# Optimization experiments

Hardware: AMD Instinct MI355X
Metric: run time of the kernel (lower is better)

## Reference

```python
import jax, jax.numpy as jnp
import numpy as np

# ---- sign binarization with straight-through estimator (standard BNN) ----
@jax.custom_vjp
def binarize(x):
    return jnp.where(x >= 0, 1.0, -1.0).astype(x.dtype)

def _bin_fwd(x):
    return binarize(x), x

def _bin_bwd(x, g):
    return (g * (jnp.abs(x) <= 1.0).astype(g.dtype),)

binarize.defvjp(_bin_fwd, _bin_bwd)

def conv2d(x, w):
    # x: [N,C,H,W], w: [O,I,kh,kw], stride 1, VALID padding (padding=0)
    return jax.lax.conv_general_dilated(
        x, w, window_strides=(1, 1), padding='VALID',
        dimension_numbers=('NCHW', 'OIHW', 'NCHW'))

def maxpool2(x):
    return jax.lax.reduce_window(x, -jnp.inf, jax.lax.max,
                                 (1, 1, 2, 2), (1, 1, 2, 2), 'VALID')

def hardtanh(x):
    return jnp.clip(x, -1.0, 1.0)

def setup_inputs() -> dict:
    key = jax.random.key(0)
    ks = jax.random.split(key, 11)
    B = 8192
    s = 0.1
    return {
        'x':   jax.random.normal(ks[0], (B, 3, 32, 32), jnp.float32),
        'w1':  jax.random.normal(ks[1], (6, 3, 5, 5), jnp.float32) * s,
        'b1':  jax.random.normal(ks[2], (6,), jnp.float32) * s,
        'w2':  jax.random.normal(ks[3], (16, 6, 5, 5), jnp.float32) * s,
        'b2':  jax.random.normal(ks[4], (16,), jnp.float32) * s,
        'wf1': jax.random.normal(ks[5], (120, 400), jnp.float32) * s,
        'bf1': jax.random.normal(ks[6], (120,), jnp.float32) * s,
        'wf2': jax.random.normal(ks[7], (84, 120), jnp.float32) * s,
        'bf2': jax.random.normal(ks[8], (84,), jnp.float32) * s,
        'wf3': jax.random.normal(ks[9], (10, 84), jnp.float32) * s,
        'bf3': jax.random.normal(ks[10], (10,), jnp.float32) * s,
    }

def reference(x, w1, b1, w2, b2, wf1, bf1, wf2, bf2, wf3, bf3):
    # conv1: first layer -> real-valued input, binarized weights
    out = conv2d(x, binarize(w1)) + b1[None, :, None, None]   # [B,6,28,28]
    out = maxpool2(hardtanh(out))                              # [B,6,14,14]
    # conv2: binarized input and weights
    out = conv2d(binarize(out), binarize(w2)) + b2[None, :, None, None]  # [B,16,10,10]
    out = maxpool2(hardtanh(out))                              # [B,16,5,5]
    out = out.reshape(out.shape[0], -1)                        # [B,400]
    out = hardtanh(binarize(out) @ binarize(wf1).T + bf1)      # [B,120]
    out = hardtanh(binarize(out) @ binarize(wf2).T + bf2)      # [B,84]
    out = binarize(out) @ binarize(wf3).T + bf3                # [B,10]
    return out
```

## Files before the change

kernel.cpp:

```cpp
#include <hip/hip_runtime.h>
#include <stdint.h>

#define TPB 256
#define RCAP 128
#define BAND 0.05f

#define WS_BFR   0
#define WS_W1B   1280
#define WS_W2PK  1298
#define WS_WF1P  1378
#define WS_WF2PK 4378
#define WS_WF3PK 4714

typedef _Float16 half8 __attribute__((ext_vector_type(8)));
typedef float f32x4 __attribute__((ext_vector_type(4)));
typedef unsigned int u32x4 __attribute__((ext_vector_type(4)));

__device__ __forceinline__ uint32_t pkf16(float a, float b) {
  uint32_t lo = (uint32_t)__builtin_bit_cast(uint16_t, (_Float16)a);
  uint32_t hi = (uint32_t)__builtin_bit_cast(uint16_t, (_Float16)b);
  return lo | (hi << 16);
}

__device__ __forceinline__ double win_sum(const float* __restrict__ xb,
                                          uint32_t b0, uint32_t b1, uint32_t b2) {
  double s = 0.0;
#pragma unroll
  for (int ic = 0; ic < 3; ++ic)
#pragma unroll
    for (int rr = 0; rr < 5; ++rr) {
      const float* rp = xb + ic * 1024 + rr * 32;
#pragma unroll
      for (int kc = 0; kc < 5; ++kc) {
        const int idx = ic * 25 + rr * 5 + kc;
        const uint32_t bw = (idx < 32) ? b0 : ((idx < 64) ? b1 : b2);
        double xv = (double)rp[kc];
        s += ((bw >> (idx & 31)) & 1u) ? xv : -xv;
      }
    }
  return s;
}

__global__ __launch_bounds__(TPB) void prep_kernel(
    const float* __restrict__ w1, const float* __restrict__ w2,
    const float* __restrict__ wf1, const float* __restrict__ wf2,
    const float* __restrict__ wf3, uint32_t* __restrict__ wsu)
{
  int id = blockIdx.x * TPB + threadIdx.x;
  if (id < 1280) {
    int s = id >> 8, r = id & 255, ln = r >> 2, dw = r & 3;
    int g4 = ln >> 4, n = ln & 15;
    int o = 4 * s + g4, r6 = o / 3, cp = o % 3;
    int c = n >> 1, dy = n & 1;
    uint32_t w = 0;
    for (int h = 0; h < 2; ++h) {
      int j2 = dw * 2 + h;
      int ic = j2 & 3, pix = j2 >> 2, kc = cp * 2 + pix, kr = r6 - dy;
      uint32_t f = 0;
      if (n < 12 && o < 18 && ic < 3 && kc < 5 && kr >= 0 && kr <= 4)
        f = (w1[(c * 3 + ic) * 25 + kr * 5 + kc] >= 0.f) ? 0x3C00u : 0xBC00u;
      w |= f << (16 * h);
    }
    wsu[WS_BFR + id] = w;
  } else if (id < 1298) {
    int i = id - 1280, c = i / 3, q = i % 3;
    uint32_t w = 0;
    for (int b = 0; b < 32; ++b) {
      int k = q * 32 + b;
      if (k < 75) w |= (uint32_t)(w1[c*75 + k] >= 0.f) << b;
    }
    wsu[WS_W1B + i] = w;
  } else if (id < 1378) {
    int r = id - 1298, oc = r / 5, kr = r % 5;
    uint32_t w = 0;
    for (int c = 0; c < 6; ++c)
      for (int k = 0; k < 5; ++k)
        w |= (uint32_t)(w2[((oc*6 + c)*5 + kr)*5 + k] >= 0.f) << (5*c + k);
    wsu[WS_W2PK + r] = w;
  } else if (id < 4378) {
    int r = id - 1378, o = r / 25, p = r % 25;
    uint32_t w = 0;
    for (int oc = 0; oc < 16; ++oc)
      w |= (uint32_t)(wf1[o*400 + oc*25 + p] >= 0.f) << oc;
    wsu[WS_WF1P + r] = w;
  } else if (id < 4714) {
    int r = id - 4378, o = r / 4, q = r % 4;
    uint32_t w = 0;
    for (int b = 0; b < 32; ++b) {
      int n = q*32 + b;
      if (n < 120) w |= (uint32_t)(wf2[o*120 + n] >= 0.f) << b;
    }
    wsu[WS_WF2PK + r] = w;
  } else if (id < 4744) {
    int r = id - 4714, o = r / 3, q = r % 3;
    uint32_t w = 0;
    for (int b = 0; b < 32; ++b) {
      int n = q*32 + b;
      if (n < 84) w |= (uint32_t)(wf3[o*84 + n] >= 0.f) << b;
    }
    wsu[WS_WF3PK + r] = w;
  }
}

__global__ void __launch_bounds__(TPB, 4) lenet_kernel(
    const float* __restrict__ x,
    const float* __restrict__ b1, const float* __restrict__ b2,
    const float* __restrict__ bf1, const float* __restrict__ bf2,
    const float* __restrict__ bf3,
    const uint32_t* __restrict__ wsu,
    float* __restrict__ out, int imgs_total)
{
  __shared__ __align__(16) union Ovl {
    uint32_t imgh[8448];
    uint32_t ppatch[4][10][10][5];
  } ovl;
  __shared__ uint32_t w1bs[18];
  __shared__ float sb1[6];
  __shared__ float sb2[16];
  __shared__ uint32_t bits1[4][6][14];
  __shared__ uint32_t border_[4][6][14];
  __shared__ uint32_t w2pks[16][5];
  __shared__ uint32_t bits2[4][25];
  __shared__ uint32_t wf2pks[84][4];
  __shared__ uint32_t wf3pks[10][3];
  __shared__ uint32_t bitsf1[4][4];
  __shared__ uint32_t bitsf2[4][3];
  __shared__ uint32_t rlist[RCAP];
  __shared__ int rcnt;

  const int t = threadIdx.x;
  const int lane = t & 63;
  const int wv = t >> 6;
  const int m16 = lane & 15;
  const int g4 = lane >> 4;
  const long long img0 = (long long)blockIdx.x * 4;
  const int nimg = (img0 + 4 <= imgs_total) ? 4 : (int)(imgs_total - img0);

  {
    const int im = t >> 6, y = (t >> 1) & 31, xh = t & 1;
    if (im < nimg) {
      const float* rp = x + (img0 + im) * 3072 + y * 32 + xh * 16;
      const int pixbase = (im * 32 + y) * 33 + xh * 16;
#pragma unroll
      for (int q = 0; q < 4; ++q) {
        float4 f0 = *(const float4*)(rp +    0 + 4 * q);
        float4 f1 = *(const float4*)(rp + 1024 + 4 * q);
        float4 f2 = *(const float4*)(rp + 2048 + 4 * q);
        uint32_t* d = &ovl.imgh[2 * (pixbase + 4 * q)];
        *(uint2*)(d + 0) = make_uint2(pkf16(f0.x, f1.x), pkf16(f2.x, 0.f));
        *(uint2*)(d + 2) = make_uint2(pkf16(f0.y, f1.y), pkf16(f2.y, 0.f));
        *(uint2*)(d + 4) = make_uint2(pkf16(f0.z, f1.z), pkf16(f2.z, 0.f));
        *(uint2*)(d + 6) = make_uint2(pkf16(f0.w, f1.w), pkf16(f2.w, 0.f));
      }
    }
    for (int id = t; id < 128; id += TPB) {
      int i2 = id >> 5, yy = id & 31;
      *(uint2*)&ovl.imgh[2 * ((i2 * 32 + yy) * 33 + 32)] = make_uint2(0u, 0u);
    }
    if (t < 18) w1bs[t] = wsu[WS_W1B + t];
    if (t < 6)  sb1[t] = b1[t];
    if (t >= 8 && t < 24) sb2[t - 8] = b2[t - 8];
    if (t < 80) w2pks[t / 5][t % 5] = wsu[WS_W2PK + t];
    if (t < 168) {
      ((uint32_t*)wf2pks)[t]       = wsu[WS_WF2PK + t];
      ((uint32_t*)wf2pks)[t + 168] = wsu[WS_WF2PK + t + 168];
    }
    if (t < 30) ((uint32_t*)wf3pks)[t] = wsu[WS_WF3PK + t];
    for (int id = t; id < 336; id += TPB) {
      ((uint32_t*)bits1)[id] = 0; ((uint32_t*)border_)[id] = 0;
    }
    if (t < 100) ((uint32_t*)bits2)[t] = 0;
    if (t < 16) ((uint32_t*)bitsf1)[t] = 0;
    if (t < 12) ((uint32_t*)bitsf2)[t] = 0;
    if (t == 0) rcnt = 0;
  }
  __syncthreads();

  if (wv < nimg) {
    u32x4 bf[5];
#pragma unroll
    for (int s = 0; s < 5; ++s)
      bf[s] = *(const u32x4*)&wsu[WS_BFR + (s << 8) + (lane << 2)];
    int koffs[5];
#pragma unroll
    for (int s = 0; s < 5; ++s) {
      const int o = 4 * s + g4;
      koffs[s] = (o < 18) ? (o / 3) * 33 + (o % 3) * 2 : 0;
    }
    const int n = m16;
    const int c = n >> 1;
    const float bcr = sb1[(n < 12) ? c : 0];
    for (int pyi = 0; pyi < 14; ++pyi) {
      const int rowpix = (wv * 32 + 2 * pyi) * 33 + m16;
      f32x4 aX = {0.f, 0.f, 0.f, 0.f}, aY = {0.f, 0.f, 0.f, 0.f};
#pragma unroll
      for (int s = 0; s < 5; ++s) {
        const uint2* pX = (const uint2*)&ovl.imgh[2 * (rowpix + koffs[s])];
        const uint2* pY = (const uint2*)&ovl.imgh[2 * (rowpix + 12 + koffs[s])];
        uint2 x0 = pX[0], x1 = pX[1];
        uint2 y0 = pY[0], y1 = pY[1];
        u32x4 wa = {x0.x, x0.y, x1.x, x1.y};
        u32x4 wb = {y0.x, y0.y, y1.x, y1.y};
        aX = __builtin_amdgcn_mfma_f32_16x16x32_f16(
               __builtin_bit_cast(half8, wa), __builtin_bit_cast(half8, bf[s]), aX, 0, 0, 0);
        aY = __builtin_amdgcn_mfma_f32_16x16x32_f16(
               __builtin_bit_cast(half8, wb), __builtin_bit_cast(half8, bf[s]), aY, 0, 0, 0);
      }
      float pX0 = fmaxf(aX[0], aX[1]), pX1 = fmaxf(aX[2], aX[3]);
      float pY0 = fmaxf(aY[0], aY[1]), pY1 = fmaxf(aY[2], aY[3]);
      float qX0 = fmaxf(pX0, __shfl_xor(pX0, 1));
      float qX1 = fmaxf(pX1, __shfl_xor(pX1, 1));
      float qY0 = fmaxf(pY0, __shfl_xor(pY0, 1));
      float qY1 = fmaxf(pY1, __shfl_xor(pY1, 1));
      uint32_t comb = 0;
      {
        float v0 = qX0 + bcr, v1 = qX1 + bcr, v2 = qY0 + bcr, v3 = qY1 + bcr;
        const int p0 = g4 * 2, p1 = g4 * 2 + 1, p2 = 6 + g4 * 2, p3 = 7 + g4 * 2;
        if (fabsf(v0) < BAND) comb |= 1u << (16 + p0); else if (v0 >= 0.f) comb |= 1u << p0;
        if (fabsf(v1) < BAND) comb |= 1u << (16 + p1); else if (v1 >= 0.f) comb |= 1u << p1;
        if (fabsf(v2) < BAND) comb |= 1u << (16 + p2); else if (v2 >= 0.f) comb |= 1u << p2;
        if (fabsf(v3) < BAND) comb |= 1u << (16 + p3); else if (v3 >= 0.f) comb |= 1u << p3;
      }
      comb |= __shfl_xor(comb, 16);
      comb |= __shfl_xor(comb, 32);
      if (g4 == 0 && n < 12 && (n & 1) == 0) {
        bits1[wv][c][pyi]   = comb & 0x3FFFu;
        border_[wv][c][pyi] = comb >> 16;
      }
    }
  }
  __syncthreads();

  for (int id = t; id < 336; id += TPB) {
    uint32_t bw = ((uint32_t*)border_)[id];
    while (bw) {
      int pj = __ffs(bw) - 1;
      bw &= bw - 1;
      int slot = atomicAdd(&rcnt, 1);
      if (slot < RCAP) rlist[slot] = (uint32_t)(id * 16 + pj);
    }
  }
  __syncthreads();

  {
    const int cnt = min(rcnt, RCAP);
    for (int k = t; k < cnt * 4; k += TPB) {
      const int e = k >> 2, win = k & 3;
      const uint32_t ent = rlist[e];
      const int pj = ent & 15, w = ent >> 4;
      const int pi = w % 14, c = (w / 14) % 6, im = w / 84;
      const int dr = win >> 1, dc = win & 1;
      const float* xb = x + (img0 + im) * 3072 + (2*pi + dr) * 32 + (2*pj + dc);
      double s = win_sum(xb, w1bs[c*3], w1bs[c*3+1], w1bs[c*3+2]);
      double s1 = fmax(s, __shfl_xor(s, 1));
      double sm = fmax(s1, __shfl_xor(s1, 2));
      if (win == 0) {
        if (sm + (double)sb1[c] >= 0.0)
          atomicOr(&((uint32_t*)bits1)[w], 1u << pj);
      }
    }
    if (rcnt > RCAP) {
      for (int id = t; id < 4704; id += TPB) {
        const int w = id / 14, pj = id % 14;
        if ((((uint32_t*)border_)[w] >> pj) & 1u) {
          const int pi = w % 14, c = (w / 14) % 6, im = w / 84;
          double best = -1e300;
          for (int dr = 0; dr < 2; ++dr)
            for (int dc = 0; dc < 2; ++dc) {
              const float* xb = x + (img0 + im) * 3072 + (2*pi + dr) * 32 + (2*pj + dc);
              double s = win_sum(xb, w1bs[c*3], w1bs[c*3+1], w1bs[c*3+2]);
              best = best > s ? best : s;
            }
          if (best + (double)sb1[c] >= 0.0)
            atomicOr(&((uint32_t*)bits1)[w], 1u << pj);
        }
      }
    }
  }
  __syncthreads();

  for (int id = t; id < 2000; id += TPB) {
    const int im  = id / 500;
    const int rem = id % 500;
    const int kr = rem % 5;
    const int ij = rem / 5;
    const int i = ij / 10, j = ij % 10;
    uint32_t w = 0;
#pragma unroll
    for (int c = 0; c < 6; ++c)
      w |= ((bits1[im][c][i + kr] >> j) & 31u) << (5*c);
    ovl.ppatch[im][i][j][kr] = w;
  }
  __syncthreads();

  for (int id = t; id < 1600; id += TPB) {
    const int im  = id / 400;
    const int rem = id % 400;
    const int oc  = rem / 25;
    const int pos = rem % 25;
    const int pi = pos / 5, pj = pos % 5;
    int dmin = 1000;
#pragma unroll
    for (int dy = 0; dy < 2; ++dy)
#pragma unroll
      for (int dx = 0; dx < 2; ++dx) {
        const uint32_t* pp = ovl.ppatch[im][2*pi + dy][2*pj + dx];
        int d = 0;
#pragma unroll
        for (int kr = 0; kr < 5; ++kr) d += __popc(pp[kr] ^ w2pks[oc][kr]);
        dmin = min(dmin, d);
      }
    float v = (float)(150 - 2*dmin) + sb2[oc];
    if (v >= 0.f) atomicOr(&bits2[im][pos], 1u << oc);
  }
  __syncthreads();

  for (int id = t; id < 480; id += TPB) {
    const int im = id / 120;
    const int o = id % 120;
    const uint32_t* wrow = wsu + WS_WF1P + o*25;
    int d = 0;
#pragma unroll
    for (int p = 0; p < 25; ++p) d += __popc(bits2[im][p] ^ wrow[p]);
    float v = (float)(400 - 2*d) + bf1[o];
    if (v >= 0.f) atomicOr(&bitsf1[im][o >> 5], 1u << (o & 31));
  }
  __syncthreads();

  for (int id = t; id < 336; id += TPB) {
    const int im = id / 84;
    const int o = id % 84;
    int d = 0;
#pragma unroll
    for (int q = 0; q < 4; ++q) d += __popc(bitsf1[im][q] ^ wf2pks[o][q]);
    float v = (float)(120 - 2*d) + bf2[o];
    if (v >= 0.f) atomicOr(&bitsf2[im][o >> 5], 1u << (o & 31));
  }
  __syncthreads();

  for (int id = t; id < 40; id += TPB) {
    const int im = id / 10;
    const int o = id % 10;
    if (im < nimg) {
      int d = 0;
#pragma unroll
      for (int q = 0; q < 3; ++q) d += __popc(bitsf2[im][q] ^ wf3pks[o][q]);
      out[(img0 + im)*10 + o] = (float)(84 - 2*d) + bf3[o];
    }
  }
}

extern "C" void kernel_launch(void* const* d_in, const int* in_sizes, int n_in,
                              void* d_out, int out_size, void* d_ws, size_t ws_size,
                              hipStream_t stream)
{
  const float* x   = (const float*)d_in[0];
  const float* w1  = (const float*)d_in[1];
  const float* b1  = (const float*)d_in[2];
  const float* w2  = (const float*)d_in[3];
  const float* b2  = (const float*)d_in[4];
  const float* wf1 = (const float*)d_in[5];
  const float* bf1 = (const float*)d_in[6];
  const float* wf2 = (const float*)d_in[7];
  const float* bf2 = (const float*)d_in[8];
  const float* wf3 = (const float*)d_in[9];
  const float* bf3 = (const float*)d_in[10];
  uint32_t* wsu = (uint32_t*)d_ws;

  const int imgs = in_sizes[0] / 3072;
  hipLaunchKernelGGL(prep_kernel, dim3(19), dim3(TPB), 0, stream,
                     w1, w2, wf1, wf2, wf3, wsu);
  const int nblk = (imgs + 3) / 4;
  hipLaunchKernelGGL(lenet_kernel, dim3(nblk), dim3(TPB), 0, stream,
                     x, b1, b2, bf1, bf2, bf3, wsu, (float*)d_out, imgs);
}
```

Measured before the change: 69.91 us.

## Process one image per 64-thread block instead of four per 256-thread block

Restructures the LeNet kernel so each block is a single wavefront handling one image, shrinking shared memory per block and launching one block per image. The aim is lighter, independent blocks with cheaper barriers and higher occupancy, instead of four wavefronts synchronising across four images. It also stops staging the FC2/FC3 packed weights in shared memory and reads them directly from global memory. The cost is more blocks, with per-block setup such as loading MFMA weight fragments repeated for every image, and fewer threads for the later popcount stages.

```diff
diff --git a/kernel.cpp b/kernel.cpp
--- a/kernel.cpp
+++ b/kernel.cpp
@@ -1,8 +1,8 @@
 #include <hip/hip_runtime.h>
 #include <stdint.h>
 
-#define TPB 256
-#define RCAP 128
+#define TPB 64
+#define RCAP 64
 #define BAND 0.05f
 
 #define WS_BFR   0
@@ -41,12 +41,12 @@
   return s;
 }
 
-__global__ __launch_bounds__(TPB) void prep_kernel(
+__global__ __launch_bounds__(256) void prep_kernel(
     const float* __restrict__ w1, const float* __restrict__ w2,
     const float* __restrict__ wf1, const float* __restrict__ wf2,
     const float* __restrict__ wf3, uint32_t* __restrict__ wsu)
 {
-  int id = blockIdx.x * TPB + threadIdx.x;
+  int id = blockIdx.x * 256 + threadIdx.x;
   if (id < 1280) {
     int s = id >> 8, r = id & 255, ln = r >> 2, dw = r & 3;
     int g4 = ln >> 4, n = ln & 15;
@@ -108,90 +108,77 @@
     const float* __restrict__ bf1, const float* __restrict__ bf2,
     const float* __restrict__ bf3,
     const uint32_t* __restrict__ wsu,
-    float* __restrict__ out, int imgs_total)
+    float* __restrict__ out)
 {
   __shared__ __align__(16) union Ovl {
-    uint32_t imgh[8448];
-    uint32_t ppatch[4][10][10][5];
+    uint32_t imgh[2112];
+    uint32_t ppatch[10][10][5];
   } ovl;
+  __shared__ uint32_t w2pks[16][5];
   __shared__ uint32_t w1bs[18];
   __shared__ float sb1[6];
   __shared__ float sb2[16];
-  __shared__ uint32_t bits1[4][6][14];
-  __shared__ uint32_t border_[4][6][14];
-  __shared__ uint32_t w2pks[16][5];
-  __shared__ uint32_t bits2[4][25];
-  __shared__ uint32_t wf2pks[84][4];
-  __shared__ uint32_t wf3pks[10][3];
-  __shared__ uint32_t bitsf1[4][4];
-  __shared__ uint32_t bitsf2[4][3];
+  __shared__ uint32_t bits1[6][14];
+  __shared__ uint32_t border_[6][14];
+  __shared__ uint32_t bits2[25];
+  __shared__ uint32_t bitsf1[4];
+  __shared__ uint32_t bitsf2[3];
   __shared__ uint32_t rlist[RCAP];
   __shared__ int rcnt;
 
   const int t = threadIdx.x;
-  const int lane = t & 63;
-  const int wv = t >> 6;
-  const int m16 = lane & 15;
-  const int g4 = lane >> 4;
-  const long long img0 = (long long)blockIdx.x * 4;
-  const int nimg = (img0 + 4 <= imgs_total) ? 4 : (int)(imgs_total - img0);
+  const int m16 = t & 15;
+  const int g4 = t >> 4;
+  const long long img = blockIdx.x;
+
+  u32x4 bf[5];
+#pragma unroll
+  for (int s = 0; s < 5; ++s)
+    bf[s] = *(const u32x4*)&wsu[WS_BFR + (s << 8) + (t << 2)];
+  int koffs[5];
+#pragma unroll
+  for (int s = 0; s < 5; ++s) {
+    const int o = 4 * s + g4;
+    koffs[s] = (o < 18) ? (o / 3) * 33 + (o % 3) * 2 : 0;
+  }
 
   {
-    const int im = t >> 6, y = (t >> 1) & 31, xh = t & 1;
-    if (im < nimg) {
-      const float* rp = x + (img0 + im) * 3072 + y * 32 + xh * 16;
-      const int pixbase = (im * 32 + y) * 33 + xh * 16;
-#pragma unroll
-      for (int q = 0; q < 4; ++q) {
-        float4 f0 = *(const float4*)(rp +    0 + 4 * q);
-        float4 f1 = *(const float4*)(rp + 1024 + 4 * q);
-        float4 f2 = *(const float4*)(rp + 2048 + 4 * q);
-        uint32_t* d = &ovl.imgh[2 * (pixbase + 4 * q)];
-        *(uint2*)(d + 0) = make_uint2(pkf16(f0.x, f1.x), pkf16(f2.x, 0.f));
-        *(uint2*)(d + 2) = make_uint2(pkf16(f0.y, f1.y), pkf16(f2.y, 0.f));
-        *(uint2*)(d + 4) = make_uint2(pkf16(f0.z, f1.z), pkf16(f2.z, 0.f));
-        *(uint2*)(d + 6) = make_uint2(pkf16(f0.w, f1.w), pkf16(f2.w, 0.f));
-      }
-    }
-    for (int id = t; id < 128; id += TPB) {
-      int i2 = id >> 5, yy = id & 31;
-      *(uint2*)&ovl.imgh[2 * ((i2 * 32 + yy) * 33 + 32)] = make_uint2(0u, 0u);
-    }
+    const int y = t >> 1, xh = t & 1;
+    const float* rp = x + img * 3072 + y * 32 + xh * 16;
+    const int pixbase = y * 33 + xh * 16;
+#pragma unroll
+    for (int q = 0; q < 4; ++q) {
+      float4 f0 = *(const float4*)(rp +    0 + 4 * q);
+      float4 f1 = *(const float4*)(rp + 1024 + 4 * q);
+      float4 f2 = *(const float4*)(rp + 2048 + 4 * q);
+      uint32_t* d = &ovl.imgh[2 * (pixbase + 4 * q)];
+      *(uint2*)(d + 0) = make_uint2(pkf16(f0.x, f1.x), pkf16(f2.x, 0.f));
+      *(uint2*)(d + 2) = make_uint2(pkf16(f0.y, f1.y), pkf16(f2.y, 0.f));
+      *(uint2*)(d + 4) = make_uint2(pkf16(f0.z, f1.z), pkf16(f2.z, 0.f));
+      *(uint2*)(d + 6) = make_uint2(pkf16(f0.w, f1.w), pkf16(f2.w, 0.f));
+    }
+    if (t < 32)
+      *(uint2*)&ovl.imgh[2 * (t * 33 + 32)] = make_uint2(0u, 0u);
+    for (int id = t; id < 80; id += TPB) w2pks[id / 5][id % 5] = wsu[WS_W2PK + id];
     if (t < 18) w1bs[t] = wsu[WS_W1B + t];
     if (t < 6)  sb1[t] = b1[t];
-    if (t >= 8 && t < 24) sb2[t - 8] = b2[t - 8];
-    if (t < 80) w2pks[t / 5][t % 5] = wsu[WS_W2PK + t];
-    if (t < 168) {
-      ((uint32_t*)wf2pks)[t]       = wsu[WS_WF2PK + t];
-      ((uint32_t*)wf2pks)[t + 168] = wsu[WS_WF2PK + t + 168];
-    }
-    if (t < 30) ((uint32_t*)wf3pks)[t] = wsu[WS_WF3PK + t];
-    for (int id = t; id < 336; id += TPB) {
+    if (t >= 32 && t < 48) sb2[t - 32] = b2[t - 32];
+    for (int id = t; id < 84; id += TPB) {
       ((uint32_t*)bits1)[id] = 0; ((uint32_t*)border_)[id] = 0;
     }
-    if (t < 100) ((uint32_t*)bits2)[t] = 0;
-    if (t < 16) ((uint32_t*)bitsf1)[t] = 0;
-    if (t < 12) ((uint32_t*)bitsf2)[t] = 0;
-    if (t == 0) rcnt = 0;
-  }
-  __syncthreads();
-
-  if (wv < nimg) {
-    u32x4 bf[5];
-#pragma unroll
-    for (int s = 0; s < 5; ++s)
-      bf[s] = *(const u32x4*)&wsu[WS_BFR + (s << 8) + (lane << 2)];
-    int koffs[5];
-#pragma unroll
-    for (int s = 0; s < 5; ++s) {
-      const int o = 4 * s + g4;
-      koffs[s] = (o < 18) ? (o / 3) * 33 + (o % 3) * 2 : 0;
-    }
+    if (t < 25) bits2[t] = 0;
+    if (t >= 25 && t < 29) bitsf1[t - 25] = 0;
+    if (t >= 29 && t < 32) bitsf2[t - 29] = 0;
+    if (t == 63) rcnt = 0;
+  }
+  __syncthreads();
+
+  {
     const int n = m16;
     const int c = n >> 1;
     const float bcr = sb1[(n < 12) ? c : 0];
     for (int pyi = 0; pyi < 14; ++pyi) {
-      const int rowpix = (wv * 32 + 2 * pyi) * 33 + m16;
+      const int rowpix = (2 * pyi) * 33 + m16;
       f32x4 aX = {0.f, 0.f, 0.f, 0.f}, aY = {0.f, 0.f, 0.f, 0.f};
 #pragma unroll
       for (int s = 0; s < 5; ++s) {
@@ -224,14 +211,14 @@
       comb |= __shfl_xor(comb, 16);
       comb |= __shfl_xor(comb, 32);
       if (g4 == 0 && n < 12 && (n & 1) == 0) {
-        bits1[wv][c][pyi]   = comb & 0x3FFFu;
-        border_[wv][c][pyi] = comb >> 16;
-      }
-    }
-  }
-  __syncthreads();
-
-  for (int id = t; id < 336; id += TPB) {
+        bits1[c][pyi]   = comb & 0x3FFFu;
+        border_[c][pyi] = comb >> 16;
+      }
+    }
+  }
+  __syncthreads();
+
+  for (int id = t; id < 84; id += TPB) {
     uint32_t bw = ((uint32_t*)border_)[id];
     while (bw) {
       int pj = __ffs(bw) - 1;
@@ -248,9 +235,9 @@
       const int e = k >> 2, win = k & 3;
       const uint32_t ent = rlist[e];
       const int pj = ent & 15, w = ent >> 4;
-      const int pi = w % 14, c = (w / 14) % 6, im = w / 84;
+      const int pi = w % 14, c = w / 14;
       const int dr = win >> 1, dc = win & 1;
-      const float* xb = x + (img0 + im) * 3072 + (2*pi + dr) * 32 + (2*pj + dc);
+      const float* xb = x + img * 3072 + (2*pi + dr) * 32 + (2*pj + dc);
       double s = win_sum(xb, w1bs[c*3], w1bs[c*3+1], w1bs[c*3+2]);
       double s1 = fmax(s, __shfl_xor(s, 1));
       double sm = fmax(s1, __shfl_xor(s1, 2));
@@ -260,14 +247,14 @@
       }
     }
     if (rcnt > RCAP) {
-      for (int id = t; id < 4704; id += TPB) {
+      for (int id = t; id < 1176; id += TPB) {
         const int w = id / 14, pj = id % 14;
         if ((((uint32_t*)border_)[w] >> pj) & 1u) {
-          const int pi = w % 14, c = (w / 14) % 6, im = w / 84;
+          const int pi = w % 14, c = w / 14;
           double best = -1e300;
           for (int dr = 0; dr < 2; ++dr)
             for (int dc = 0; dc < 2; ++dc) {
-              const float* xb = x + (img0 + im) * 3072 + (2*pi + dr) * 32 + (2*pj + dc);
+              const float* xb = x + img * 3072 + (2*pi + dr) * 32 + (2*pj + dc);
               double s = win_sum(xb, w1bs[c*3], w1bs[c*3+1], w1bs[c*3+2]);
               best = best > s ? best : s;
             }
@@ -279,74 +266,67 @@
   }
   __syncthreads();
 
-  for (int id = t; id < 2000; id += TPB) {
-    const int im  = id / 500;
-    const int rem = id % 500;
-    const int kr = rem % 5;
-    const int ij = rem / 5;
+  for (int id = t; id < 500; id += TPB) {
+    const int kr = id % 5;
+    const int ij = id / 5;
     const int i = ij / 10, j = ij % 10;
     uint32_t w = 0;
 #pragma unroll
     for (int c = 0; c < 6; ++c)
-      w |= ((bits1[im][c][i + kr] >> j) & 31u) << (5*c);
-    ovl.ppatch[im][i][j][kr] = w;
-  }
-  __syncthreads();
-
-  for (int id = t; id < 1600; id += TPB) {
-    const int im  = id / 400;
-    const int rem = id % 400;
-    const int oc  = rem / 25;
-    const int pos = rem % 25;
+      w |= ((bits1[c][i + kr] >> j) & 31u) << (5*c);
+    ovl.ppatch[i][j][kr] = w;
+  }
+  __syncthreads();
+
+  for (int id = t; id < 400; id += TPB) {
+    const int oc  = id / 25;
+    const int pos = id % 25;
     const int pi = pos / 5, pj = pos % 5;
     int dmin = 1000;
 #pragma unroll
     for (int dy = 0; dy < 2; ++dy)
 #pragma unroll
       for (int dx = 0; dx < 2; ++dx) {
-        const uint32_t* pp = ovl.ppatch[im][2*pi + dy][2*pj + dx];
+        const uint32_t* pp = ovl.ppatch[2*pi + dy][2*pj + dx];
         int d = 0;
 #pragma unroll
         for (int kr = 0; kr < 5; ++kr) d += __popc(pp[kr] ^ w2pks[oc][kr]);
         dmin = min(dmin, d);
       }
     float v = (float)(150 - 2*dmin) + sb2[oc];
-    if (v >= 0.f) atomicOr(&bits2[im][pos], 1u << oc);
-  }
-  __syncthreads();
-
-  for (int id = t; id < 480; id += TPB) {
-    const int im = id / 120;
-    const int o = id % 120;
+    if (v >= 0.f) atomicOr(&bits2[pos], 1u << oc);
+  }
+  __syncthreads();
+
+  for (int id = t; id < 120; id += TPB) {
+    const int o = id;
     const uint32_t* wrow = wsu + WS_WF1P + o*25;
     int d = 0;
 #pragma unroll
-    for (int p = 0; p < 25; ++p) d += __popc(bits2[im][p] ^ wrow[p]);
+    for (int p = 0; p < 25; ++p) d += __popc(bits2[p] ^ wrow[p]);
     float v = (float)(400 - 2*d) + bf1[o];
-    if (v >= 0.f) atomicOr(&bitsf1[im][o >> 5], 1u << (o & 31));
-  }
-  __syncthreads();
-
-  for (int id = t; id < 336; id += TPB) {
-    const int im = id / 84;
-    const int o = id % 84;
+    if (v >= 0.f) atomicOr(&bitsf1[o >> 5], 1u << (o & 31));
+  }
+  __syncthreads();
+
+  for (int id = t; id < 84; id += TPB) {
+    const int o = id;
     int d = 0;
 #pragma unroll
-    for (int q = 0; q < 4; ++q) d += __popc(bitsf1[im][q] ^ wf2pks[o][q]);
+    for (int q = 0; q < 4; ++q)
+      d += __popc(bitsf1[q] ^ wsu[WS_WF2PK + o*4 + q]);
     float v = (float)(120 - 2*d) + bf2[o];
-    if (v >= 0.f) atomicOr(&bitsf2[im][o >> 5], 1u << (o & 31));
-  }
-  __syncthreads();
-
-  for (int id = t; id < 40; id += TPB) {
-    const int im = id / 10;
-    const int o = id % 10;
-    if (im < nimg) {
-      int d = 0;
-#pragma unroll
-      for (int q = 0; q < 3; ++q) d += __popc(bitsf2[im][q] ^ wf3pks[o][q]);
-      out[(img0 + im)*10 + o] = (float)(84 - 2*d) + bf3[o];
-    }
+    if (v >= 0.f) atomicOr(&bitsf2[o >> 5], 1u << (o & 31));
+  }
+  __syncthreads();
+
+  if (t < 10) {
+    const int o = t;
+    int d = 0;
+#pragma unroll
+    for (int q = 0; q < 3; ++q)
+      d += __popc(bitsf2[q] ^ wsu[WS_WF3PK + o*3 + q]);
+    out[img*10 + o] = (float)(84 - 2*d) + bf3[o];
   }
 }
 
@@ -368,9 +348,8 @@
   uint32_t* wsu = (uint32_t*)d_ws;
 
   const int imgs = in_sizes[0] / 3072;
-  hipLaunchKernelGGL(prep_kernel, dim3(19), dim3(TPB), 0, stream,
+  hipLaunchKernelGGL(prep_kernel, dim3(19), dim3(256), 0, stream,
                      w1, w2, wf1, wf2, wf3, wsu);
-  const int nblk = (imgs + 3) / 4;
-  hipLaunchKernelGGL(lenet_kernel, dim3(nblk), dim3(TPB), 0, stream,
-                     x, b1, b2, bf1, bf2, bf3, wsu, (float*)d_out, imgs);
-}
+  hipLaunchKernelGGL(lenet_kernel, dim3(imgs), dim3(TPB), 0, stream,
+                     x, b1, b2, bf1, bf2, bf3, wsu, (float*)d_out);
+}
```

Measured after the change: 67.16 us. 1.04x faster.
